# Performance work log

Measured on AMD Instinct MI355X. Metric: run time of the kernel, lower is better.

The kernel has to match this reference:

```python
import jax, jax.numpy as jnp
import numpy as np

DIM = 768
NUM_HEADS = 12
HEAD_DIM = DIM // NUM_HEADS
SCALE = HEAD_DIM ** (-0.5)


def setup_inputs() -> dict:
    key = jax.random.key(0)
    ks = jax.random.split(key, 8)
    B, Nq, Nk, Nv = 2, 2048, 2048, 2048
    init = 0.02
    return {
        "xq": jax.random.normal(ks[0], (B, Nq, DIM), dtype=jnp.float32),
        "xk": jax.random.normal(ks[1], (B, Nk, DIM), dtype=jnp.float32),
        "xv": jax.random.normal(ks[2], (B, Nv, DIM), dtype=jnp.float32),
        # torch nn.Linear weights are [out_features, in_features]; qkv_bias=False
        "Wq": jax.random.normal(ks[3], (DIM, DIM), dtype=jnp.float32) * init,
        "Wk": jax.random.normal(ks[4], (DIM, DIM), dtype=jnp.float32) * init,
        "Wv": jax.random.normal(ks[5], (DIM, DIM), dtype=jnp.float32) * init,
        "Wp": jax.random.normal(ks[6], (DIM, DIM), dtype=jnp.float32) * init,
        "bp": jax.random.normal(ks[7], (DIM,), dtype=jnp.float32) * init,
    }


def reference(xq, xk, xv, Wq, Wk, Wv, Wp, bp):
    B, Nq, C = xq.shape
    H, D = NUM_HEADS, HEAD_DIM
    # linear projections (torch Linear: x @ W.T), split heads -> [B, H, N, D]
    q = (xq @ Wq.T).reshape(B, Nq, H, D).transpose(0, 2, 1, 3)
    k = (xk @ Wk.T).reshape(B, xk.shape[1], H, D).transpose(0, 2, 1, 3)
    v = (xv @ Wv.T).reshape(B, xv.shape[1], H, D).transpose(0, 2, 1, 3)
    # attention scores [B, H, Nq, Nk]
    attn = jnp.einsum("bhqd,bhkd->bhqk", q, k) * SCALE
    attn = jax.nn.softmax(attn, axis=-1)
    # weighted values -> merge heads [B, Nq, C]
    out = jnp.einsum("bhqk,bhkd->bhqd", attn, v)
    out = out.transpose(0, 2, 1, 3).reshape(B, Nq, C)
    return out @ Wp.T + bp
```

## Files before the change

### kernel.cpp

```cpp
#include <hip/hip_runtime.h>
#include <hip/hip_bf16.h>


#define NSEQ 2048
#define CDIM 768
#define NH   12
#define HD   64
#define MTOT 4096
#define XEL  (MTOT*CDIM)
#define WEL  (CDIM*CDIM)
#define X8   (XEL/8)
#define W8   (WEL/8)
#define QSCALE 0.18033688011112042f

typedef __attribute__((ext_vector_type(8))) short bf16x8;
typedef __attribute__((ext_vector_type(4))) float floatx4;
typedef __attribute__((ext_vector_type(16))) float floatx16;
typedef __attribute__((ext_vector_type(4))) unsigned int uintx4;

static __device__ __forceinline__ unsigned short f2bf(float f) {
  union { float f; unsigned int u; } v; v.f = f;
  return (unsigned short)((v.u + 0x8000u) >> 16);
}
static __device__ __forceinline__ unsigned pk2bf(float a, float b) {
  unsigned ua = __float_as_uint(a) + 0x8000u;
  unsigned ub = __float_as_uint(b) + 0x8000u;
  return __builtin_amdgcn_perm(ub, ua, 0x07060302);
}
static __device__ __forceinline__ unsigned cvtpk(float a, float b) {
  unsigned r;
  asm("v_cvt_pk_bf16_f32 %0, %1, %2" : "=v"(r) : "v"(a), "v"(b));
  return r;
}

static __device__ __forceinline__ void lds16(const void* g, void* l) {
  __builtin_amdgcn_global_load_lds(
      (const __attribute__((address_space(1))) unsigned int*)g,
      (__attribute__((address_space(3))) unsigned int*)l, 16, 0, 0);
}

#define LGKM0_SB()  do { asm volatile("s_waitcnt lgkmcnt(0)" ::: "memory"); \
                         __builtin_amdgcn_sched_barrier(0); } while (0)
#define VMCNT0()    asm volatile("s_waitcnt vmcnt(0)" ::: "memory")
#define BARRIER()   __builtin_amdgcn_s_barrier()
#define SB0()       __builtin_amdgcn_sched_barrier(0)
#define PRIO1()     __builtin_amdgcn_s_setprio(1)
#define PRIO0()     __builtin_amdgcn_s_setprio(0)

__global__ __launch_bounds__(256) void cast_all(
    const float* __restrict__ xq, const float* __restrict__ xk,
    const float* __restrict__ xv, const float* __restrict__ wq,
    const float* __restrict__ wk, const float* __restrict__ wv,
    const float* __restrict__ wp,
    unsigned short* __restrict__ Xq, unsigned short* __restrict__ Xk,
    unsigned short* __restrict__ Xv, unsigned short* __restrict__ Wq,
    unsigned short* __restrict__ Wk, unsigned short* __restrict__ Wv,
    unsigned short* __restrict__ Wp) {
  int i = blockIdx.x * 256 + threadIdx.x;
  const float* s; unsigned short* d; int off;
  if (i < 3 * X8) {
    int t = i / X8; off = i - t * X8;
    s = (t == 0) ? xq : (t == 1) ? xk : xv;
    d = (t == 0) ? Xq : (t == 1) ? Xk : Xv;
  } else {
    int j = i - 3 * X8; int t = j / W8; off = j - t * W8;
    s = (t == 0) ? wq : (t == 1) ? wk : (t == 2) ? wv : wp;
    d = (t == 0) ? Wq : (t == 1) ? Wk : (t == 2) ? Wv : Wp;
  }
  const float4* sp = (const float4*)s + (size_t)off * 2;
  float4 a = sp[0], b = sp[1];
  uint4 o;
  o.x = pk2bf(a.x, a.y); o.y = pk2bf(a.z, a.w);
  o.z = pk2bf(b.x, b.y); o.w = pk2bf(b.z, b.w);
  *(uint4*)(d + (size_t)off * 8) = o;
}

__global__ __launch_bounds__(256) void gemm_qkv(
    const unsigned short* __restrict__ Xq, const unsigned short* __restrict__ Xk,
    const unsigned short* __restrict__ Xv, const unsigned short* __restrict__ Wq,
    const unsigned short* __restrict__ Wk, const unsigned short* __restrict__ Wv,
    unsigned short* __restrict__ Qo, unsigned short* __restrict__ Ko,
    unsigned short* __restrict__ Vo) {
  int i0 = blockIdx.x;
  int mg = i0 & 7; int t0 = i0 >> 3;
  int z = t0 % 3; int u = t0 / 3;
  int xn = u & 7, ysub = u >> 3;
  int y = mg * 4 + ysub;
  const unsigned short* A; const unsigned short* B; int am0, bn0, RA;
  if (z == 0)      { A = Xq; B = Wq; am0 = y * 128; bn0 = xn * 96; RA = 128; }
  else if (z == 1) { A = Xk; B = Wk; am0 = y * 128; bn0 = xn * 96; RA = 128; }
  else             { A = Wv; B = Xv; am0 = xn * 96; bn0 = y * 128; RA = 96; }
  __shared__ __align__(16) unsigned short S[224 * 64];
  int tid = threadIdx.x, lane = tid & 63, wave = tid >> 6;
  int quad = lane >> 4, l15 = lane & 15, l7 = l15 & 7;

  const unsigned short* gptr[7]; int ldo[7];
#pragma unroll
  for (int i = 0; i < 7; i++) {
    int idx = i * 256 + tid;
    int row = idx >> 3, c = (idx & 7) ^ (row & 7);
    gptr[i] = (row < RA ? A + (size_t)(am0 + row) * CDIM
                        : B + (size_t)(bn0 + row - RA) * CDIM) + c * 8;
    ldo[i] = idx * 8;
  }
  floatx4 acc[12];
#pragma unroll
  for (int i = 0; i < 12; i++) acc[i] = (floatx4){0.f, 0.f, 0.f, 0.f};

#pragma unroll
  for (int i = 0; i < 7; i++) lds16(gptr[i], &S[ldo[i]]);
  VMCNT0();
  BARRIER();

  if (z < 2) {
    int wm = (wave >> 1) * 64, wn = (wave & 1) * 48;
    for (int k0 = 0; k0 < CDIM; k0 += 64) {
      bf16x8 af[2][4], bfr[2][3];
#pragma unroll
      for (int ks = 0; ks < 2; ks++) {
        int csw = ((ks * 4 + quad) ^ l7) * 8;
#pragma unroll
        for (int i = 0; i < 4; i++)
          af[ks][i] = *(const bf16x8*)&S[(wm + i * 16 + l15) * 64 + csw];
#pragma unroll
        for (int j = 0; j < 3; j++)
          bfr[ks][j] = *(const bf16x8*)&S[(128 + wn + j * 16 + l15) * 64 + csw];
      }
      LGKM0_SB();
      BARRIER();
      if (k0 + 64 < CDIM) {
#pragma unroll
        for (int i = 0; i < 7; i++) lds16(gptr[i] + k0 + 64, &S[ldo[i]]);
      }
      SB0();
      PRIO1();
#pragma unroll
      for (int ks = 0; ks < 2; ks++)
#pragma unroll
        for (int mi = 0; mi < 4; mi++)
#pragma unroll
          for (int ni = 0; ni < 3; ni++)
            acc[mi * 3 + ni] = __builtin_amdgcn_mfma_f32_16x16x32_bf16(
                af[ks][mi], bfr[ks][ni], acc[mi * 3 + ni], 0, 0, 0);
      PRIO0();
      VMCNT0();
      BARRIER();
    }
#pragma unroll
    for (int mi = 0; mi < 4; mi++)
#pragma unroll
      for (int ni = 0; ni < 3; ni++)
#pragma unroll
        for (int r = 0; r < 4; r++) {
          int grow = am0 + wm + mi * 16 + quad * 4 + r;
          int gcol = bn0 + wn + ni * 16 + l15;
          float v = acc[mi * 3 + ni][r];
          int b = grow >> 11, nq = grow & 2047, h = gcol >> 6, dd = gcol & 63;
          if (z == 0)
            Qo[((size_t)(b * NH + h) * NSEQ + nq) * HD + dd] = f2bf(v * QSCALE);
          else
            Ko[((size_t)(b * NH + h) * NSEQ + nq) * HD + dd] = f2bf(v);
        }
  } else {
    int wm = (wave & 1) * 48, wn = (wave >> 1) * 64;
    for (int k0 = 0; k0 < CDIM; k0 += 64) {
      bf16x8 af[2][3], bfr[2][4];
#pragma unroll
      for (int ks = 0; ks < 2; ks++) {
        int csw = ((ks * 4 + quad) ^ l7) * 8;
#pragma unroll
        for (int i = 0; i < 3; i++)
          af[ks][i] = *(const bf16x8*)&S[(wm + i * 16 + l15) * 64 + csw];
#pragma unroll
        for (int j = 0; j < 4; j++)
          bfr[ks][j] = *(const bf16x8*)&S[(96 + wn + j * 16 + l15) * 64 + csw];
      }
      LGKM0_SB();
      BARRIER();
      if (k0 + 64 < CDIM) {
#pragma unroll
        for (int i = 0; i < 7; i++) lds16(gptr[i] + k0 + 64, &S[ldo[i]]);
      }
      SB0();
      PRIO1();
#pragma unroll
      for (int ks = 0; ks < 2; ks++)
#pragma unroll
        for (int mi = 0; mi < 3; mi++)
#pragma unroll
          for (int ni = 0; ni < 4; ni++)
            acc[mi * 4 + ni] = __builtin_amdgcn_mfma_f32_16x16x32_bf16(
                af[ks][mi], bfr[ks][ni], acc[mi * 4 + ni], 0, 0, 0);
      PRIO0();
      VMCNT0();
      BARRIER();
    }
#pragma unroll
    for (int mi = 0; mi < 3; mi++)
#pragma unroll
      for (int ni = 0; ni < 4; ni++)
#pragma unroll
        for (int r = 0; r < 4; r++) {
          int o = am0 + wm + mi * 16 + quad * 4 + r;
          int mgl = bn0 + wn + ni * 16 + l15;
          int b = mgl >> 11, nq = mgl & 2047;
          Vo[((size_t)b * CDIM + o) * NSEQ + nq] = f2bf(acc[mi * 4 + ni][r]);
        }
  }
}

__global__ __launch_bounds__(256, 3) void attn_kernel(
    const unsigned short* __restrict__ Q, const unsigned short* __restrict__ K,
    const unsigned short* __restrict__ Vt, unsigned short* __restrict__ ctx) {
  int i0 = blockIdx.x;
  int xcd = i0 & 7; int t0 = i0 >> 3;
  int bh = xcd * 3 + (t0 >> 5);
  int qt = t0 & 31;
  int tid = threadIdx.x, lane = tid & 63, wave = tid >> 6;
  int half = wave >> 1, qsub = wave & 1;
  int l31 = lane & 31, hi = lane >> 5;
  __shared__ __align__(16) unsigned short Ks[2][64 * 64];
  __shared__ __align__(16) unsigned short Vs[2][64 * 64];
  __shared__ float Lbuf[64];

  const unsigned short* Qg = Q + ((size_t)bh * NSEQ + qt * 64 + qsub * 32) * HD;
  const unsigned short* Kg = K + ((size_t)bh * NSEQ + half * 1024) * HD;
  const unsigned short* Vg = Vt + (size_t)bh * HD * NSEQ + half * 1024;

  bf16x8 qf[4];
#pragma unroll
  for (int dc = 0; dc < 4; dc++)
    qf[dc] = *(const bf16x8*)(Qg + l31 * HD + dc * 16 + hi * 8);

  int tid2 = tid & 127;
  int kgo[4], vgo[4], ldst[4];
#pragma unroll
  for (int i = 0; i < 4; i++) {
    int idx = i * 128 + tid2;
    int R = idx >> 3, c = (idx & 7) ^ (R & 7);
    kgo[i] = R * HD + c * 8;
    vgo[i] = R * NSEQ + c * 8;
    ldst[i] = idx * 8;
  }
  unsigned short* Ksh = Ks[half];
  unsigned short* Vsh = Vs[half];

  floatx16 o[2];
#pragma unroll
  for (int dt = 0; dt < 2; dt++) o[dt] = (floatx16)(0.f);
  float l_acc = 0.f;

#pragma unroll
  for (int i = 0; i < 4; i++) {
    lds16(Kg + kgo[i], &Ksh[ldst[i]]);
    lds16(Vg + vgo[i], &Vsh[ldst[i]]);
  }
  VMCNT0();
  BARRIER();

  for (int t = 0; t < 16; t++) {
    bf16x8 kf[2][4];
#pragma unroll
    for (int kb = 0; kb < 2; kb++)
#pragma unroll
      for (int dc = 0; dc < 4; dc++) {
        int R = kb * 32 + l31, c = dc * 2 + hi;
        kf[kb][dc] = *(const bf16x8*)&Ksh[R * 64 + ((c ^ (R & 7)) * 8)];
      }
    bf16x8 vf[2][4];
#pragma unroll
    for (int dt = 0; dt < 2; dt++)
#pragma unroll
      for (int j = 0; j < 4; j++) {
        int R = dt * 32 + l31, c = j * 2 + hi;
        vf[dt][j] = *(const bf16x8*)&Vsh[R * 64 + ((c ^ (R & 7)) * 8)];
      }
    LGKM0_SB();
    BARRIER();
    if (t < 15) {
      int k0n = (t + 1) * 64;
#pragma unroll
      for (int i = 0; i < 4; i++) {
        lds16(Kg + (size_t)k0n * HD + kgo[i], &Ksh[ldst[i]]);
        lds16(Vg + k0n + vgo[i], &Vsh[ldst[i]]);
      }
    }
    SB0();
#pragma unroll
    for (int kb = 0; kb < 2; kb++) {
      floatx16 st = (floatx16)(0.f);
      PRIO1();
#pragma unroll
      for (int dc = 0; dc < 4; dc++)
        st = __builtin_amdgcn_mfma_f32_32x32x16_bf16(kf[kb][dc], qf[dc], st, 0, 0, 0);
      PRIO0();
      float p[16];
#pragma unroll
      for (int r = 0; r < 16; r++) p[r] = __builtin_exp2f(st[r]);
      l_acc += ((p[0] + p[1]) + (p[2] + p[3])) + ((p[4] + p[5]) + (p[6] + p[7])) +
               (((p[8] + p[9]) + (p[10] + p[11])) + ((p[12] + p[13]) + (p[14] + p[15])));
      unsigned w[8];
#pragma unroll
      for (int i = 0; i < 8; i++) w[i] = cvtpk(p[2 * i], p[2 * i + 1]);
#pragma unroll
      for (int kvs = 0; kvs < 2; kvs++) {
        unsigned a0 = w[kvs * 4 + 0], b0 = w[kvs * 4 + 2];
        unsigned a1 = w[kvs * 4 + 1], b1 = w[kvs * 4 + 3];
        asm volatile("v_permlane32_swap_b32 %0, %1" : "+v"(a0), "+v"(b0));
        asm volatile("v_permlane32_swap_b32 %0, %1" : "+v"(a1), "+v"(b1));
        uintx4 pw; pw[0] = a0; pw[1] = a1; pw[2] = b0; pw[3] = b1;
        bf16x8 pb = *(bf16x8*)&pw;
        PRIO1();
#pragma unroll
        for (int dt = 0; dt < 2; dt++)
          o[dt] = __builtin_amdgcn_mfma_f32_32x32x16_bf16(
              vf[dt][kb * 2 + kvs], pb, o[dt], 0, 0, 0);
        PRIO0();
      }
    }
    VMCNT0();
    BARRIER();
  }

  unsigned lu = __float_as_uint(l_acc), lv = __float_as_uint(l_acc);
  asm volatile("v_permlane32_swap_b32 %0, %1" : "+v"(lu), "+v"(lv));
  float lfull = __uint_as_float(lu) + __uint_as_float(lv);

  float* Obuf = (float*)&Ks[0][0];
  int q = qsub * 32 + l31;
  if (half == 1) {
#pragma unroll
    for (int dt = 0; dt < 2; dt++)
#pragma unroll
      for (int rq = 0; rq < 4; rq++) {
        int ch = (dt * 8 + rq * 2 + hi) ^ (l31 & 15);
        floatx4 v4 = {o[dt][rq * 4 + 0], o[dt][rq * 4 + 1],
                      o[dt][rq * 4 + 2], o[dt][rq * 4 + 3]};
        *(floatx4*)&Obuf[q * 64 + ch * 4] = v4;
      }
    if (lane < 32) Lbuf[qsub * 32 + lane] = lfull;
  }
  __syncthreads();
  if (half == 0) {
    int b = bh / NH, h = bh - b * NH;
    float inv = 1.f / (lfull + Lbuf[q]);
    int qrow = qt * 64 + q;
#pragma unroll
    for (int dt = 0; dt < 2; dt++)
#pragma unroll
      for (int rq = 0; rq < 4; rq++) {
        int ch = (dt * 8 + rq * 2 + hi) ^ (l31 & 15);
        floatx4 ob = *(floatx4*)&Obuf[q * 64 + ch * 4];
        float v0 = (o[dt][rq * 4 + 0] + ob[0]) * inv;
        float v1 = (o[dt][rq * 4 + 1] + ob[1]) * inv;
        float v2 = (o[dt][rq * 4 + 2] + ob[2]) * inv;
        float v3 = (o[dt][rq * 4 + 3] + ob[3]) * inv;
        size_t gbase = (size_t)(b * NSEQ + qrow) * CDIM + h * HD +
                       dt * 32 + rq * 8 + hi * 4;
        *(uint2*)&ctx[gbase] = make_uint2(pk2bf(v0, v1), pk2bf(v2, v3));
      }
  }
}

__global__ __launch_bounds__(256) void gemm_out(
    const unsigned short* __restrict__ A, const unsigned short* __restrict__ B,
    const float* __restrict__ bias, float* __restrict__ out) {
  int i0 = blockIdx.x;
  int mg = i0 & 7; int t0 = i0 >> 3;
  int n0 = (t0 & 7) * 96;
  int m0 = (mg * 8 + (t0 >> 3)) * 64;
  __shared__ __align__(16) unsigned short S[160 * 128];
  int tid = threadIdx.x, lane = tid & 63, wave = tid >> 6;
  int quad = lane >> 4, l15 = lane & 15, l7 = l15 & 7;
  int wm = (wave >> 1) * 32, wn = (wave & 1) * 48;
  floatx4 acc[6];
#pragma unroll
  for (int i = 0; i < 6; i++) acc[i] = (floatx4){0.f, 0.f, 0.f, 0.f};

  int sro[10]; const unsigned short* sgp[10];
#pragma unroll
  for (int i = 0; i < 10; i++) {
    int idx = i * 256 + tid;
    int R = idx >> 4, c4 = idx & 15;
    int cs = (c4 & 8) | ((c4 & 7) ^ (R & 7));
    sgp[i] = ((R < 64) ? A + (size_t)(m0 + R) * CDIM
                       : B + (size_t)(n0 + R - 64) * CDIM) + cs * 8;
    sro[i] = idx * 8;
  }
#pragma unroll
  for (int i = 0; i < 10; i++) lds16(sgp[i], &S[sro[i]]);
  VMCNT0();
  BARRIER();

  for (int k0 = 0; k0 < CDIM; k0 += 128) {
    bf16x8 af[4][2], bfr[4][3];
#pragma unroll
    for (int ks = 0; ks < 4; ks++) {
      int c = ks * 4 + quad;
      int csw = ((c & 8) | ((c & 7) ^ l7)) * 8;
#pragma unroll
      for (int i = 0; i < 2; i++)
        af[ks][i] = *(const bf16x8*)&S[(wm + i * 16 + l15) * 128 + csw];
#pragma unroll
      for (int j = 0; j < 3; j++)
        bfr[ks][j] = *(const bf16x8*)&S[(64 + wn + j * 16 + l15) * 128 + csw];
    }
    LGKM0_SB();
    BARRIER();
    if (k0 + 128 < CDIM) {
#pragma unroll
      for (int i = 0; i < 10; i++) lds16(sgp[i] + k0 + 128, &S[sro[i]]);
    }
    SB0();
    PRIO1();
#pragma unroll
    for (int ks = 0; ks < 4; ks++)
#pragma unroll
      for (int mi = 0; mi < 2; mi++)
#pragma unroll
        for (int ni = 0; ni < 3; ni++)
          acc[mi * 3 + ni] = __builtin_amdgcn_mfma_f32_16x16x32_bf16(
              af[ks][mi], bfr[ks][ni], acc[mi * 3 + ni], 0, 0, 0);
    PRIO0();
    VMCNT0();
    BARRIER();
  }
  float bv[3];
#pragma unroll
  for (int ni = 0; ni < 3; ni++) bv[ni] = bias[n0 + wn + ni * 16 + l15];
#pragma unroll
  for (int mi = 0; mi < 2; mi++)
#pragma unroll
    for (int ni = 0; ni < 3; ni++)
#pragma unroll
      for (int r = 0; r < 4; r++) {
        int grow = m0 + wm + mi * 16 + quad * 4 + r;
        int gcol = n0 + wn + ni * 16 + l15;
        out[(size_t)grow * CDIM + gcol] = acc[mi * 3 + ni][r] + bv[ni];
      }
}

extern "C" void kernel_launch(void* const* d_in, const int* in_sizes, int n_in,
                              void* d_out, int out_size, void* d_ws, size_t ws_size,
                              hipStream_t stream) {
  const float* xq = (const float*)d_in[0];
  const float* xk = (const float*)d_in[1];
  const float* xv = (const float*)d_in[2];
  const float* wq = (const float*)d_in[3];
  const float* wk = (const float*)d_in[4];
  const float* wv = (const float*)d_in[5];
  const float* wp = (const float*)d_in[6];
  const float* bp = (const float*)d_in[7];
  float* out = (float*)d_out;

  char* p = (char*)d_ws;
  unsigned short* Xq = (unsigned short*)p; p += (size_t)XEL * 2;
  unsigned short* Xk = (unsigned short*)p; p += (size_t)XEL * 2;
  unsigned short* Xv = (unsigned short*)p; p += (size_t)XEL * 2;
  unsigned short* Wq = (unsigned short*)p; p += (size_t)WEL * 2;
  unsigned short* Wk = (unsigned short*)p; p += (size_t)WEL * 2;
  unsigned short* Wv = (unsigned short*)p; p += (size_t)WEL * 2;
  unsigned short* Wp = (unsigned short*)p; p += (size_t)WEL * 2;
  unsigned short* Qb = (unsigned short*)p; p += (size_t)XEL * 2;
  unsigned short* Kb = (unsigned short*)p; p += (size_t)XEL * 2;
  unsigned short* Vb = (unsigned short*)p; p += (size_t)XEL * 2;
  unsigned short* Cx = (unsigned short*)p; p += (size_t)XEL * 2;

  cast_all<<<(3 * X8 + 4 * W8) / 256, 256, 0, stream>>>(
      xq, xk, xv, wq, wk, wv, wp, Xq, Xk, Xv, Wq, Wk, Wv, Wp);

  gemm_qkv<<<768, 256, 0, stream>>>(
      Xq, Xk, Xv, Wq, Wk, Wv, Qb, Kb, Vb);

  attn_kernel<<<768, 256, 0, stream>>>(Qb, Kb, Vb, Cx);

  gemm_out<<<512, 256, 0, stream>>>(Cx, Wp, bp, out);
}
```

Baseline: 173.2 us.

## Interleave QK MFMAs across key blocks and retile output GEMM to 64x64

In the attention inner loop, the two QK^T score MFMA chains for both 32-key sub-blocks are now interleaved and their exponentials computed together before the PV MFMAs. This gives the MFMA pipeline two independent accumulators and more instruction-level parallelism, at the cost of extra registers. The output projection GEMM goes from 64x96 tiles (512 blocks) to 64x64 tiles (768 blocks) to fill more CUs, with less reuse per block.

```diff
diff --git a/kernel.cpp b/kernel.cpp
--- a/kernel.cpp
+++ b/kernel.cpp
@@ -286,26 +286,41 @@
       }
     }
     SB0();
-#pragma unroll
-    for (int kb = 0; kb < 2; kb++) {
-      floatx16 st = (floatx16)(0.f);
-      PRIO1();
-#pragma unroll
-      for (int dc = 0; dc < 4; dc++)
-        st = __builtin_amdgcn_mfma_f32_32x32x16_bf16(kf[kb][dc], qf[dc], st, 0, 0, 0);
-      PRIO0();
-      float p[16];
-#pragma unroll
-      for (int r = 0; r < 16; r++) p[r] = __builtin_exp2f(st[r]);
-      l_acc += ((p[0] + p[1]) + (p[2] + p[3])) + ((p[4] + p[5]) + (p[6] + p[7])) +
-               (((p[8] + p[9]) + (p[10] + p[11])) + ((p[12] + p[13]) + (p[14] + p[15])));
-      unsigned w[8];
-#pragma unroll
-      for (int i = 0; i < 8; i++) w[i] = cvtpk(p[2 * i], p[2 * i + 1]);
+    floatx16 st0 = (floatx16)(0.f), st1 = (floatx16)(0.f);
+    PRIO1();
+#pragma unroll
+    for (int dc = 0; dc < 4; dc++) {
+      st0 = __builtin_amdgcn_mfma_f32_32x32x16_bf16(kf[0][dc], qf[dc], st0, 0, 0, 0);
+      st1 = __builtin_amdgcn_mfma_f32_32x32x16_bf16(kf[1][dc], qf[dc], st1, 0, 0, 0);
+    }
+    PRIO0();
+    float p[32];
+#pragma unroll
+    for (int r = 0; r < 16; r++) {
+      p[r] = __builtin_exp2f(st0[r]);
+      p[16 + r] = __builtin_exp2f(st1[r]);
+    }
+    {
+      float u0 = (p[0] + p[1]) + (p[2] + p[3]);
+      float u1 = (p[4] + p[5]) + (p[6] + p[7]);
+      float u2 = (p[8] + p[9]) + (p[10] + p[11]);
+      float u3 = (p[12] + p[13]) + (p[14] + p[15]);
+      float u4 = (p[16] + p[17]) + (p[18] + p[19]);
+      float u5 = (p[20] + p[21]) + (p[22] + p[23]);
+      float u6 = (p[24] + p[25]) + (p[26] + p[27]);
+      float u7 = (p[28] + p[29]) + (p[30] + p[31]);
+      l_acc += ((u0 + u1) + (u2 + u3)) + ((u4 + u5) + (u6 + u7));
+    }
+    unsigned w[16];
+#pragma unroll
+    for (int i = 0; i < 16; i++) w[i] = cvtpk(p[2 * i], p[2 * i + 1]);
+#pragma unroll
+    for (int kb = 0; kb < 2; kb++)
 #pragma unroll
       for (int kvs = 0; kvs < 2; kvs++) {
-        unsigned a0 = w[kvs * 4 + 0], b0 = w[kvs * 4 + 2];
-        unsigned a1 = w[kvs * 4 + 1], b1 = w[kvs * 4 + 3];
+        int base = kb * 8 + kvs * 4;
+        unsigned a0 = w[base + 0], b0 = w[base + 2];
+        unsigned a1 = w[base + 1], b1 = w[base + 3];
         asm volatile("v_permlane32_swap_b32 %0, %1" : "+v"(a0), "+v"(b0));
         asm volatile("v_permlane32_swap_b32 %0, %1" : "+v"(a1), "+v"(b1));
         uintx4 pw; pw[0] = a0; pw[1] = a1; pw[2] = b0; pw[3] = b1;
@@ -317,7 +332,6 @@
               vf[dt][kb * 2 + kvs], pb, o[dt], 0, 0, 0);
         PRIO0();
       }
-    }
     VMCNT0();
     BARRIER();
   }
@@ -367,19 +381,19 @@
     const float* __restrict__ bias, float* __restrict__ out) {
   int i0 = blockIdx.x;
   int mg = i0 & 7; int t0 = i0 >> 3;
-  int n0 = (t0 & 7) * 96;
-  int m0 = (mg * 8 + (t0 >> 3)) * 64;
-  __shared__ __align__(16) unsigned short S[160 * 128];
+  int n0 = (t0 % 12) * 64;
+  int m0 = (mg * 8 + (t0 / 12)) * 64;
+  __shared__ __align__(16) unsigned short S[128 * 128];
   int tid = threadIdx.x, lane = tid & 63, wave = tid >> 6;
   int quad = lane >> 4, l15 = lane & 15, l7 = l15 & 7;
-  int wm = (wave >> 1) * 32, wn = (wave & 1) * 48;
-  floatx4 acc[6];
-#pragma unroll
-  for (int i = 0; i < 6; i++) acc[i] = (floatx4){0.f, 0.f, 0.f, 0.f};
-
-  int sro[10]; const unsigned short* sgp[10];
-#pragma unroll
-  for (int i = 0; i < 10; i++) {
+  int wm = (wave >> 1) * 32, wn = (wave & 1) * 32;
+  floatx4 acc[4];
+#pragma unroll
+  for (int i = 0; i < 4; i++) acc[i] = (floatx4){0.f, 0.f, 0.f, 0.f};
+
+  int sro[8]; const unsigned short* sgp[8];
+#pragma unroll
+  for (int i = 0; i < 8; i++) {
     int idx = i * 256 + tid;
     int R = idx >> 4, c4 = idx & 15;
     int cs = (c4 & 8) | ((c4 & 7) ^ (R & 7));
@@ -388,12 +402,12 @@
     sro[i] = idx * 8;
   }
 #pragma unroll
-  for (int i = 0; i < 10; i++) lds16(sgp[i], &S[sro[i]]);
+  for (int i = 0; i < 8; i++) lds16(sgp[i], &S[sro[i]]);
   VMCNT0();
   BARRIER();
 
   for (int k0 = 0; k0 < CDIM; k0 += 128) {
-    bf16x8 af[4][2], bfr[4][3];
+    bf16x8 af[4][2], bfr[4][2];
 #pragma unroll
     for (int ks = 0; ks < 4; ks++) {
       int c = ks * 4 + quad;
@@ -402,14 +416,14 @@
       for (int i = 0; i < 2; i++)
         af[ks][i] = *(const bf16x8*)&S[(wm + i * 16 + l15) * 128 + csw];
 #pragma unroll
-      for (int j = 0; j < 3; j++)
+      for (int j = 0; j < 2; j++)
         bfr[ks][j] = *(const bf16x8*)&S[(64 + wn + j * 16 + l15) * 128 + csw];
     }
     LGKM0_SB();
     BARRIER();
     if (k0 + 128 < CDIM) {
 #pragma unroll
-      for (int i = 0; i < 10; i++) lds16(sgp[i] + k0 + 128, &S[sro[i]]);
+      for (int i = 0; i < 8; i++) lds16(sgp[i] + k0 + 128, &S[sro[i]]);
     }
     SB0();
     PRIO1();
@@ -418,25 +432,25 @@
 #pragma unroll
       for (int mi = 0; mi < 2; mi++)
 #pragma unroll
-        for (int ni = 0; ni < 3; ni++)
-          acc[mi * 3 + ni] = __builtin_amdgcn_mfma_f32_16x16x32_bf16(
-              af[ks][mi], bfr[ks][ni], acc[mi * 3 + ni], 0, 0, 0);
+        for (int ni = 0; ni < 2; ni++)
+          acc[mi * 2 + ni] = __builtin_amdgcn_mfma_f32_16x16x32_bf16(
+              af[ks][mi], bfr[ks][ni], acc[mi * 2 + ni], 0, 0, 0);
     PRIO0();
     VMCNT0();
     BARRIER();
   }
-  float bv[3];
-#pragma unroll
-  for (int ni = 0; ni < 3; ni++) bv[ni] = bias[n0 + wn + ni * 16 + l15];
+  float bv[2];
+#pragma unroll
+  for (int ni = 0; ni < 2; ni++) bv[ni] = bias[n0 + wn + ni * 16 + l15];
 #pragma unroll
   for (int mi = 0; mi < 2; mi++)
 #pragma unroll
-    for (int ni = 0; ni < 3; ni++)
+    for (int ni = 0; ni < 2; ni++)
 #pragma unroll
       for (int r = 0; r < 4; r++) {
         int grow = m0 + wm + mi * 16 + quad * 4 + r;
         int gcol = n0 + wn + ni * 16 + l15;
-        out[(size_t)grow * CDIM + gcol] = acc[mi * 3 + ni][r] + bv[ni];
+        out[(size_t)grow * CDIM + gcol] = acc[mi * 2 + ni][r] + bv[ni];
       }
 }
 
@@ -474,5 +488,5 @@
 
   attn_kernel<<<768, 256, 0, stream>>>(Qb, Kb, Vb, Cx);
 
-  gemm_out<<<512, 256, 0, stream>>>(Cx, Wp, bp, out);
-}
+  gemm_out<<<768, 256, 0, stream>>>(Cx, Wp, bp, out);
+}
```

Result: slower. 186.1 us (+7.4%).

## Split attention KV range across two blocks with separate combine kernel

Applied to the files above, without the earlier changes.

The attention kernel becomes a split-KV pass: each query tile is handled by two blocks, each covering half of the keys, and each block iterates over 32-key sub-tiles with smaller LDS buffers, allowing higher occupancy (launch bound 6). Partial fp32 outputs and row sums go to scratch buffers that reuse the output and the cast-input workspace. A new combine kernel sums the partials, normalizes, and writes bf16 context. This is meant to raise parallelism and occupancy, at the cost of an extra launch and extra fp32 partial traffic through global memory.

```diff
diff --git a/kernel.cpp b/kernel.cpp
--- a/kernel.cpp
+++ b/kernel.cpp
@@ -209,23 +209,25 @@
   }
 }
 
-__global__ __launch_bounds__(256, 3) void attn_kernel(
+__global__ __launch_bounds__(256, 6) void attn_part(
     const unsigned short* __restrict__ Q, const unsigned short* __restrict__ K,
-    const unsigned short* __restrict__ Vt, unsigned short* __restrict__ ctx) {
+    const unsigned short* __restrict__ Vt,
+    float* __restrict__ P0, float* __restrict__ P1,
+    float* __restrict__ L0, float* __restrict__ L1) {
   int i0 = blockIdx.x;
   int xcd = i0 & 7; int t0 = i0 >> 3;
-  int bh = xcd * 3 + (t0 >> 5);
-  int qt = t0 & 31;
+  int bh = xcd * 3 + (t0 >> 6);
+  int rem = t0 & 63;
+  int qt = rem >> 1, kvh = rem & 1;
   int tid = threadIdx.x, lane = tid & 63, wave = tid >> 6;
   int half = wave >> 1, qsub = wave & 1;
   int l31 = lane & 31, hi = lane >> 5;
-  __shared__ __align__(16) unsigned short Ks[2][64 * 64];
-  __shared__ __align__(16) unsigned short Vs[2][64 * 64];
+  __shared__ __align__(16) unsigned short SM[8192];
   __shared__ float Lbuf[64];
 
   const unsigned short* Qg = Q + ((size_t)bh * NSEQ + qt * 64 + qsub * 32) * HD;
-  const unsigned short* Kg = K + ((size_t)bh * NSEQ + half * 1024) * HD;
-  const unsigned short* Vg = Vt + (size_t)bh * HD * NSEQ + half * 1024;
+  const unsigned short* Kg = K + ((size_t)bh * NSEQ + kvh * 1024 + half * 512) * HD;
+  const unsigned short* Vg = Vt + (size_t)bh * HD * NSEQ + kvh * 1024 + half * 512;
 
   bf16x8 qf[4];
 #pragma unroll
@@ -233,17 +235,17 @@
     qf[dc] = *(const bf16x8*)(Qg + l31 * HD + dc * 16 + hi * 8);
 
   int tid2 = tid & 127;
-  int kgo[4], vgo[4], ldst[4];
-#pragma unroll
-  for (int i = 0; i < 4; i++) {
+  int kgo[2], kst[2], vgo[2], vst[2];
+#pragma unroll
+  for (int i = 0; i < 2; i++) {
     int idx = i * 128 + tid2;
-    int R = idx >> 3, c = (idx & 7) ^ (R & 7);
-    kgo[i] = R * HD + c * 8;
-    vgo[i] = R * NSEQ + c * 8;
-    ldst[i] = idx * 8;
-  }
-  unsigned short* Ksh = Ks[half];
-  unsigned short* Vsh = Vs[half];
+    int Rk = idx >> 3, ck = (idx & 7) ^ (Rk & 7);
+    kgo[i] = Rk * HD + ck * 8; kst[i] = idx * 8;
+    int Rv = idx >> 2, cv = (idx & 3) ^ (Rv & 3);
+    vgo[i] = Rv * NSEQ + cv * 8; vst[i] = idx * 8;
+  }
+  unsigned short* Ksh = &SM[half * 2048];
+  unsigned short* Vsh = &SM[4096 + half * 2048];
 
   floatx16 o[2];
 #pragma unroll
@@ -251,72 +253,67 @@
   float l_acc = 0.f;
 
 #pragma unroll
-  for (int i = 0; i < 4; i++) {
-    lds16(Kg + kgo[i], &Ksh[ldst[i]]);
-    lds16(Vg + vgo[i], &Vsh[ldst[i]]);
+  for (int i = 0; i < 2; i++) {
+    lds16(Kg + kgo[i], &Ksh[kst[i]]);
+    lds16(Vg + vgo[i], &Vsh[vst[i]]);
   }
   VMCNT0();
   BARRIER();
 
   for (int t = 0; t < 16; t++) {
-    bf16x8 kf[2][4];
-#pragma unroll
-    for (int kb = 0; kb < 2; kb++)
-#pragma unroll
-      for (int dc = 0; dc < 4; dc++) {
-        int R = kb * 32 + l31, c = dc * 2 + hi;
-        kf[kb][dc] = *(const bf16x8*)&Ksh[R * 64 + ((c ^ (R & 7)) * 8)];
-      }
-    bf16x8 vf[2][4];
+    bf16x8 kf[4];
+#pragma unroll
+    for (int dc = 0; dc < 4; dc++) {
+      int c = dc * 2 + hi;
+      kf[dc] = *(const bf16x8*)&Ksh[l31 * 64 + ((c ^ (l31 & 7)) * 8)];
+    }
+    bf16x8 vf[2][2];
 #pragma unroll
     for (int dt = 0; dt < 2; dt++)
 #pragma unroll
-      for (int j = 0; j < 4; j++) {
-        int R = dt * 32 + l31, c = j * 2 + hi;
-        vf[dt][j] = *(const bf16x8*)&Vsh[R * 64 + ((c ^ (R & 7)) * 8)];
+      for (int kvs = 0; kvs < 2; kvs++) {
+        int R = dt * 32 + l31, c = kvs * 2 + hi;
+        vf[dt][kvs] = *(const bf16x8*)&Vsh[R * 32 + ((c ^ (R & 3)) * 8)];
       }
     LGKM0_SB();
     BARRIER();
     if (t < 15) {
-      int k0n = (t + 1) * 64;
-#pragma unroll
-      for (int i = 0; i < 4; i++) {
-        lds16(Kg + (size_t)k0n * HD + kgo[i], &Ksh[ldst[i]]);
-        lds16(Vg + k0n + vgo[i], &Vsh[ldst[i]]);
+      int off = (t + 1) * 32;
+#pragma unroll
+      for (int i = 0; i < 2; i++) {
+        lds16(Kg + (size_t)off * HD + kgo[i], &Ksh[kst[i]]);
+        lds16(Vg + off + vgo[i], &Vsh[vst[i]]);
       }
     }
     SB0();
-#pragma unroll
-    for (int kb = 0; kb < 2; kb++) {
-      floatx16 st = (floatx16)(0.f);
+    floatx16 st = (floatx16)(0.f);
+    PRIO1();
+#pragma unroll
+    for (int dc = 0; dc < 4; dc++)
+      st = __builtin_amdgcn_mfma_f32_32x32x16_bf16(kf[dc], qf[dc], st, 0, 0, 0);
+    PRIO0();
+    float p[16];
+#pragma unroll
+    for (int r = 0; r < 16; r++) p[r] = __builtin_exp2f(st[r]);
+    l_acc += ((p[0] + p[1]) + (p[2] + p[3])) + ((p[4] + p[5]) + (p[6] + p[7])) +
+             (((p[8] + p[9]) + (p[10] + p[11])) + ((p[12] + p[13]) + (p[14] + p[15])));
+    unsigned w[8];
+#pragma unroll
+    for (int i = 0; i < 8; i++) w[i] = cvtpk(p[2 * i], p[2 * i + 1]);
+#pragma unroll
+    for (int kvs = 0; kvs < 2; kvs++) {
+      unsigned a0 = w[kvs * 4 + 0], b0 = w[kvs * 4 + 2];
+      unsigned a1 = w[kvs * 4 + 1], b1 = w[kvs * 4 + 3];
+      asm volatile("v_permlane32_swap_b32 %0, %1" : "+v"(a0), "+v"(b0));
+      asm volatile("v_permlane32_swap_b32 %0, %1" : "+v"(a1), "+v"(b1));
+      uintx4 pw; pw[0] = a0; pw[1] = a1; pw[2] = b0; pw[3] = b1;
+      bf16x8 pb = *(bf16x8*)&pw;
       PRIO1();
 #pragma unroll
-      for (int dc = 0; dc < 4; dc++)
-        st = __builtin_amdgcn_mfma_f32_32x32x16_bf16(kf[kb][dc], qf[dc], st, 0, 0, 0);
+      for (int dt = 0; dt < 2; dt++)
+        o[dt] = __builtin_amdgcn_mfma_f32_32x32x16_bf16(
+            vf[dt][kvs], pb, o[dt], 0, 0, 0);
       PRIO0();
-      float p[16];
-#pragma unroll
-      for (int r = 0; r < 16; r++) p[r] = __builtin_exp2f(st[r]);
-      l_acc += ((p[0] + p[1]) + (p[2] + p[3])) + ((p[4] + p[5]) + (p[6] + p[7])) +
-               (((p[8] + p[9]) + (p[10] + p[11])) + ((p[12] + p[13]) + (p[14] + p[15])));
-      unsigned w[8];
-#pragma unroll
-      for (int i = 0; i < 8; i++) w[i] = cvtpk(p[2 * i], p[2 * i + 1]);
-#pragma unroll
-      for (int kvs = 0; kvs < 2; kvs++) {
-        unsigned a0 = w[kvs * 4 + 0], b0 = w[kvs * 4 + 2];
-        unsigned a1 = w[kvs * 4 + 1], b1 = w[kvs * 4 + 3];
-        asm volatile("v_permlane32_swap_b32 %0, %1" : "+v"(a0), "+v"(b0));
-        asm volatile("v_permlane32_swap_b32 %0, %1" : "+v"(a1), "+v"(b1));
-        uintx4 pw; pw[0] = a0; pw[1] = a1; pw[2] = b0; pw[3] = b1;
-        bf16x8 pb = *(bf16x8*)&pw;
-        PRIO1();
-#pragma unroll
-        for (int dt = 0; dt < 2; dt++)
-          o[dt] = __builtin_amdgcn_mfma_f32_32x32x16_bf16(
-              vf[dt][kb * 2 + kvs], pb, o[dt], 0, 0, 0);
-        PRIO0();
-      }
     }
     VMCNT0();
     BARRIER();
@@ -326,8 +323,11 @@
   asm volatile("v_permlane32_swap_b32 %0, %1" : "+v"(lu), "+v"(lv));
   float lfull = __uint_as_float(lu) + __uint_as_float(lv);
 
-  float* Obuf = (float*)&Ks[0][0];
+  float* Obuf = (float*)&SM[0];
   int q = qsub * 32 + l31;
+  int slot = bh * 32 + qt;
+  float* Pdst = (kvh == 0) ? P0 : P1;
+  float* Ldst = (kvh == 0) ? L0 : L1;
   if (half == 1) {
 #pragma unroll
     for (int dt = 0; dt < 2; dt++)
@@ -338,27 +338,49 @@
                       o[dt][rq * 4 + 2], o[dt][rq * 4 + 3]};
         *(floatx4*)&Obuf[q * 64 + ch * 4] = v4;
       }
-    if (lane < 32) Lbuf[qsub * 32 + lane] = lfull;
+    if (hi == 0) Lbuf[q] = lfull;
   }
   __syncthreads();
   if (half == 0) {
-    int b = bh / NH, h = bh - b * NH;
-    float inv = 1.f / (lfull + Lbuf[q]);
-    int qrow = qt * 64 + q;
 #pragma unroll
     for (int dt = 0; dt < 2; dt++)
 #pragma unroll
       for (int rq = 0; rq < 4; rq++) {
         int ch = (dt * 8 + rq * 2 + hi) ^ (l31 & 15);
         floatx4 ob = *(floatx4*)&Obuf[q * 64 + ch * 4];
-        float v0 = (o[dt][rq * 4 + 0] + ob[0]) * inv;
-        float v1 = (o[dt][rq * 4 + 1] + ob[1]) * inv;
-        float v2 = (o[dt][rq * 4 + 2] + ob[2]) * inv;
-        float v3 = (o[dt][rq * 4 + 3] + ob[3]) * inv;
-        size_t gbase = (size_t)(b * NSEQ + qrow) * CDIM + h * HD +
-                       dt * 32 + rq * 8 + hi * 4;
-        *(uint2*)&ctx[gbase] = make_uint2(pk2bf(v0, v1), pk2bf(v2, v3));
-      }
+        floatx4 v4 = {o[dt][rq * 4 + 0] + ob[0], o[dt][rq * 4 + 1] + ob[1],
+                      o[dt][rq * 4 + 2] + ob[2], o[dt][rq * 4 + 3] + ob[3]};
+        *(floatx4*)&Pdst[(size_t)slot * 4096 + q * 64 + dt * 32 + rq * 8 + hi * 4] = v4;
+      }
+    if (hi == 0) Ldst[slot * 64 + q] = lfull + Lbuf[q];
+  }
+}
+
+__global__ __launch_bounds__(256) void attn_combine(
+    const float* __restrict__ P0, const float* __restrict__ P1,
+    const float* __restrict__ L0, const float* __restrict__ L1,
+    unsigned short* __restrict__ ctx) {
+  int slot = blockIdx.x;
+  int bh = slot >> 5, qt = slot & 31;
+  int b = bh / NH, h = bh - b * NH;
+  int tid = threadIdx.x;
+  int e0 = tid * 16;
+  int q = e0 >> 6, d0 = e0 & 63;
+  float inv = 1.f / (L0[slot * 64 + q] + L1[slot * 64 + q]);
+  const float4* p0 = (const float4*)(P0 + (size_t)slot * 4096 + e0);
+  const float4* p1 = (const float4*)(P1 + (size_t)slot * 4096 + e0);
+  unsigned short* dst =
+      ctx + ((size_t)(b * NSEQ + qt * 64 + q)) * CDIM + h * HD + d0;
+#pragma unroll
+  for (int g = 0; g < 2; g++) {
+    float4 x0 = p0[g * 2 + 0], x1 = p0[g * 2 + 1];
+    float4 y0 = p1[g * 2 + 0], y1 = p1[g * 2 + 1];
+    uint4 ov;
+    ov.x = pk2bf((x0.x + y0.x) * inv, (x0.y + y0.y) * inv);
+    ov.y = pk2bf((x0.z + y0.z) * inv, (x0.w + y0.w) * inv);
+    ov.z = pk2bf((x1.x + y1.x) * inv, (x1.y + y1.y) * inv);
+    ov.w = pk2bf((x1.z + y1.z) * inv, (x1.w + y1.w) * inv);
+    *(uint4*)(dst + g * 8) = ov;
   }
 }
 
@@ -466,13 +488,20 @@
   unsigned short* Vb = (unsigned short*)p; p += (size_t)XEL * 2;
   unsigned short* Cx = (unsigned short*)p; p += (size_t)XEL * 2;
 
+  float* P0 = out;
+  float* P1 = (float*)Xq;
+  float* L0 = (float*)Xv;
+  float* L1 = (float*)Xv + 768 * 64;
+
   cast_all<<<(3 * X8 + 4 * W8) / 256, 256, 0, stream>>>(
       xq, xk, xv, wq, wk, wv, wp, Xq, Xk, Xv, Wq, Wk, Wv, Wp);
 
   gemm_qkv<<<768, 256, 0, stream>>>(
       Xq, Xk, Xv, Wq, Wk, Wv, Qb, Kb, Vb);
 
-  attn_kernel<<<768, 256, 0, stream>>>(Qb, Kb, Vb, Cx);
+  attn_part<<<1536, 256, 0, stream>>>(Qb, Kb, Vb, P0, P1, L0, L1);
+
+  attn_combine<<<768, 256, 0, stream>>>(P0, P1, L0, L1, Cx);
 
   gemm_out<<<512, 256, 0, stream>>>(Cx, Wp, bp, out);
 }
```

Measured after the change: 343.0 us. +98.0%, slower.
